# Optimization experiments

Measured on AMD Instinct MI355X. Metric: run time of the kernel, lower is better.

The kernel has to match this reference:

```python
import jax, jax.numpy as jnp
from jax import lax
import numpy as np

B, L_IN, L_OUT, N, COV = 16, 96, 24, 320, 4
E, H = 64, 128
CIN = E + COV


def setup_inputs() -> dict:
    key = jax.random.key(0)
    ks = jax.random.split(key, 16)
    s = 0.05
    inp = {
        'history_data': jax.random.normal(ks[0], (B, L_IN, N, 1 + COV), jnp.float32),
        'future_data': jax.random.normal(ks[1], (B, L_OUT, N, 1 + COV), jnp.float32),
        'We': jax.random.normal(ks[2], (E, 1), jnp.float32) * s,
        'be': jnp.zeros((E,), jnp.float32),
        'Wih0': jax.random.normal(ks[3], (4 * H, CIN), jnp.float32) * s,
        'Whh0': jax.random.normal(ks[4], (4 * H, H), jnp.float32) * s,
        'bih0': jnp.zeros((4 * H,), jnp.float32),
        'bhh0': jnp.zeros((4 * H,), jnp.float32),
        'Wih1': jax.random.normal(ks[5], (4 * H, H), jnp.float32) * s,
        'Whh1': jax.random.normal(ks[6], (4 * H, H), jnp.float32) * s,
        'bih1': jnp.zeros((4 * H,), jnp.float32),
        'bhh1': jnp.zeros((4 * H,), jnp.float32),
        'Wh': jax.random.normal(ks[7], (2, H), jnp.float32) * s,
        'bh': jnp.zeros((2,), jnp.float32),
        'train': 1,
    }
    return inp


def _run_layer(xs, Wih, Whh, bih, bhh):
    # xs: [T, BN, Cin] -> ys: [T, BN, H]
    h0 = jnp.zeros((xs.shape[1], Whh.shape[1]), xs.dtype)

    def step(carry, x):
        h, c = carry
        g = x @ Wih.T + bih + h @ Whh.T + bhh  # [BN, 4H]
        i, f, gg, o = jnp.split(g, 4, axis=-1)  # torch gate order i,f,g,o
        c = jax.nn.sigmoid(f) * c + jax.nn.sigmoid(i) * jnp.tanh(gg)
        h = jax.nn.sigmoid(o) * jnp.tanh(c)
        return (h, c), h

    (_, _), ys = lax.scan(step, (h0, h0), xs)
    return ys


def reference(history_data, future_data, We, be, Wih0, Whh0, bih0, bhh0,
              Wih1, Whh1, bih1, bhh1, Wh, bh, train):
    # train branch (teacher forcing): history_next is always ground truth
    T = L_IN + L_OUT
    tgt = jnp.concatenate([history_data[..., 0:1], future_data[..., 0:1]], axis=1)  # [B,T,N,1]
    cov = jnp.concatenate([history_data[..., 1:], future_data[..., 1:]], axis=1)   # [B,T,N,COV]
    # step t uses target at t-1 and covariates at t, for t = 1..T-1
    embed = tgt[:, :T - 1] @ We.T + be                       # [B,T-1,N,E]
    enc_in = jnp.concatenate([embed, cov[:, 1:T]], axis=-1)  # [B,T-1,N,CIN]
    xs = enc_in.transpose(1, 0, 2, 3).reshape(T - 1, B * N, CIN)
    ys = _run_layer(xs, Wih0, Whh0, bih0, bhh0)
    ys = _run_layer(ys, Wih1, Whh1, bih1, bhh1)
    hid = jax.nn.relu(ys)                                    # [T-1, BN, H]
    head = hid @ Wh.T + bh                                   # [T-1, BN, 2]
    mu = head[..., 0:1]
    sigma = jax.nn.softplus(head[..., 1:2])
    p = jnp.concatenate([mu, sigma], axis=-1)
    p = p[-L_OUT:].reshape(L_OUT, B, N, 2).transpose(1, 0, 2, 3)  # [B,L_out,N,2]
    return p
```

## Files before the change

### kernel.cpp

```cpp
#include <hip/hip_runtime.h>

typedef __bf16 bf16x8 __attribute__((ext_vector_type(8)));
typedef unsigned short us8 __attribute__((ext_vector_type(8)));
typedef float f32x4 __attribute__((ext_vector_type(4)));

#define NROW 32
#define A_STR 136
#define AX_STR 40
#define WL_STR 521
#define NSTEP 119

__device__ __forceinline__ unsigned short f2bf(float f){
  unsigned int x = __builtin_bit_cast(unsigned int, f);
  x += 0x7fffu + ((x >> 16) & 1u);
  return (unsigned short)(x >> 16);
}
__device__ __forceinline__ float bf2f(unsigned short s){
  unsigned int x = ((unsigned int)s) << 16;
  return __builtin_bit_cast(float, x);
}
__device__ __forceinline__ float sigm(float x){ return 1.0f/(1.0f + __expf(-x)); }
__device__ __forceinline__ float tanh_(float x){ float e = __expf(2.0f*x); return 1.0f - 2.0f/(e + 1.0f); }

__device__ __forceinline__ f32x4 MFMA(us8 a, us8 b, f32x4 c){
  return __builtin_amdgcn_mfma_f32_16x16x32_bf16(
      __builtin_bit_cast(bf16x8, a), __builtin_bit_cast(bf16x8, b), c, 0, 0, 0);
}
__device__ __forceinline__ void mfma_ag_first(f32x4& d, us8 a, us8 b){
  asm("s_nop 1\n\tv_mfma_f32_16x16x32_bf16 %0, %1, %2, %0" : "+v"(d) : "v"(a), "a"(b));
}
__device__ __forceinline__ void mfma_ag(f32x4& d, us8 a, us8 b){
  asm("v_mfma_f32_16x16x32_bf16 %0, %1, %2, %0" : "+v"(d) : "v"(a), "a"(b));
}
__device__ __forceinline__ void accfence4(f32x4& a0, f32x4& a1, f32x4& a2, f32x4& a3){
  asm("s_nop 7\n\ts_nop 7\n\ts_nop 2"
      : "+v"(a0), "+v"(a1), "+v"(a2), "+v"(a3));
}

struct SharedMem {
  unsigned short A0[2][NROW*A_STR];
  unsigned short A1[2][NROW*A_STR];
  unsigned short Ax[2][NROW][AX_STR];
  unsigned short xw[512*8];
  unsigned short W0l[8*WL_STR*8];
  float c_lds[2][2][512][4];
  float b1[512];
  float Wh2f[256];
  float red[NROW][16][2];
  float we_s[64];
  float be_s[64];
  float bh_s[2];
};

__global__ __launch_bounds__(512)
__attribute__((amdgpu_waves_per_eu(2, 2)))
void deepar_kernel(
    const float* __restrict__ hist, const float* __restrict__ fut,
    const float* __restrict__ We,   const float* __restrict__ be,
    const float* __restrict__ Wih0, const float* __restrict__ Whh0,
    const float* __restrict__ bih0, const float* __restrict__ bhh0,
    const float* __restrict__ Wih1, const float* __restrict__ Whh1,
    const float* __restrict__ bih1, const float* __restrict__ bhh1,
    const float* __restrict__ Wh,   const float* __restrict__ bh,
    float* __restrict__ out)
{
  __shared__ SharedMem S;
  const int tid = threadIdx.x;
  const int wg  = blockIdx.x;
  const int b   = wg / 10;
  const int n0  = (wg % 10) * NROW;
  const int w   = tid >> 6;
  const int l   = tid & 63;
  const int gq  = l >> 4;
  const int r   = l & 15;
  const int cw  = w * 16;

  {
    us8 z = {0,0,0,0,0,0,0,0};
    us8* pA0 = (us8*)&S.A0[0][0];
    us8* pA1 = (us8*)&S.A1[0][0];
    for (int i = tid; i < 2*NROW*A_STR/8; i += 512){ pA0[i] = z; pA1[i] = z; }
    us8* pAx = (us8*)&S.Ax[0][0][0];
    for (int i = tid; i < 2*NROW*AX_STR/8; i += 512) pAx[i] = z;
    f32x4 zf = {0.f,0.f,0.f,0.f};
    #pragma unroll
    for (int q = 0; q < 4; ++q) *(f32x4*)&S.c_lds[q >> 1][q & 1][tid][0] = zf;
  }
  if (tid < 64)       S.we_s[tid]       = We[tid];
  else if (tid < 128) S.be_s[tid - 64]  = be[tid - 64];
  else if (tid < 384) S.Wh2f[tid - 128] = Wh[tid - 128];
  else if (tid < 386) S.bh_s[tid - 384] = bh[tid - 384];
  __syncthreads();

  {
    const float* wr = Wih0 + tid * 68;
    float u = 0.f, v = 0.f;
    #pragma unroll 8
    for (int e = 0; e < 64; ++e){
      float wv = wr[e];
      u = fmaf(wv, S.we_s[e], u);
      v = fmaf(wv, S.be_s[e], v);
    }
    v += bih0[tid] + bhh0[tid];
    unsigned short* xp = &S.xw[tid * 8];
    xp[0] = f2bf(u);
    xp[1] = f2bf(wr[64]); xp[2] = f2bf(wr[65]); xp[3] = f2bf(wr[66]); xp[4] = f2bf(wr[67]);
    xp[5] = f2bf(v);
    xp[6] = 0; xp[7] = 0;
    S.b1[tid] = bih1[tid] + bhh1[tid];
  }
  for (int idx = tid; idx < 8*512; idx += 512){
    int qgq = idx >> 9, col = idx & 511;
    const float* p = Whh0 + col*128 + qgq*8;
    f32x4 x0 = *(const f32x4*)p;
    f32x4 x1 = *(const f32x4*)(p + 4);
    us8 tt;
    tt[0]=f2bf(x0[0]); tt[1]=f2bf(x0[1]); tt[2]=f2bf(x0[2]); tt[3]=f2bf(x0[3]);
    tt[4]=f2bf(x1[0]); tt[5]=f2bf(x1[1]); tt[6]=f2bf(x1[2]); tt[7]=f2bf(x1[3]);
    *(us8*)&S.W0l[(qgq*WL_STR + col)*8] = tt;
  }
  if (tid < 64){ int row = tid >> 1, bsel = tid & 1; S.Ax[bsel][row][5] = 0x3F80; }
  if (tid < 160){
    int srow, sch, tau;
    if (tid < 32){ srow = tid; sch = 0; tau = 0; }
    else { int k = tid - 32; srow = k >> 2; sch = 1 + (k & 3); tau = 1; }
    const float* p = hist + ((b*96 + tau)*320 + n0 + srow)*5;
    S.Ax[0][srow][sch] = f2bf(p[sch]);
  }

  us8 WV[4][2], WA1[4][4], WA2[4][4];
  #pragma unroll
  for (int m = 0; m < 3; ++m){
    const float* base = (m == 0) ? Whh0 : (m == 1) ? Wih1 : Whh1;
    #pragma unroll
    for (int g = 0; g < 4; ++g){
      int col = g*128 + cw + r;
      #pragma unroll
      for (int q = 0; q < 4; ++q){
        if (m == 0 && q < 2) continue;
        const float* p = base + col*128 + q*32 + gq*8;
        f32x4 x0 = *(const f32x4*)p;
        f32x4 x1 = *(const f32x4*)(p + 4);
        us8 tt;
        tt[0]=f2bf(x0[0]); tt[1]=f2bf(x0[1]); tt[2]=f2bf(x0[2]); tt[3]=f2bf(x0[3]);
        tt[4]=f2bf(x1[0]); tt[5]=f2bf(x1[1]); tt[6]=f2bf(x1[2]); tt[7]=f2bf(x1[3]);
        if (m == 0)      WV[g][q-2] = tt;
        else if (m == 1) WA1[g][q]  = tt;
        else             WA2[g][q]  = tt;
      }
    }
  }

  __syncthreads();

  float b1g[4];
  #pragma unroll
  for (int g = 0; g < 4; ++g) b1g[g] = S.b1[g*128 + cw + r];

  for (int t = 0; t < NSTEP; ++t){
    const int pb = t & 1, nb = pb ^ 1;
    const unsigned short* A0r = S.A0[pb];
    unsigned short*       A0w = S.A0[nb];
    const unsigned short* A1r = S.A1[pb];
    unsigned short*       A1w = S.A1[nb];

    float stv = 0.f; int sto = -1;
    if (t + 1 < NSTEP && tid < 160){
      int srow, sch, tau;
      if (tid < 32){ srow = tid; sch = 0; tau = t + 1; }
      else { int k = tid - 32; srow = k >> 2; sch = 1 + (k & 3); tau = t + 2; }
      const float* p = (tau < 96) ? (hist + ((b*96 + tau)*320 + n0 + srow)*5)
                                  : (fut  + ((b*24 + (tau - 96))*320 + n0 + srow)*5);
      stv = p[sch];
      sto = nb*NROW*AX_STR + srow*AX_STR + sch;
    }

    #pragma unroll
    for (int rt = 0; rt < 2; ++rt){
      const int rbase = rt * 16;
      f32x4 acc[4];
      us8 ax = *(const us8*)&S.Ax[pb][rbase + r][gq*8];
      #pragma unroll
      for (int g = 0; g < 4; ++g){
        us8 bx = *(const us8*)&S.xw[(g*128 + cw + r)*8];
        f32x4 z = {0.f,0.f,0.f,0.f};
        acc[g] = MFMA(ax, bx, z);
      }
      #pragma unroll
      for (int q = 0; q < 2; ++q){
        us8 a = *(const us8*)&A0r[(rbase + r)*A_STR + q*32 + gq*8];
        #pragma unroll
        for (int g = 0; g < 4; ++g){
          us8 bw = *(const us8*)&S.W0l[((q*4 + gq)*WL_STR + g*128 + cw + r)*8];
          acc[g] = MFMA(a, bw, acc[g]);
        }
      }
      #pragma unroll
      for (int q = 2; q < 4; ++q){
        us8 a = *(const us8*)&A0r[(rbase + r)*A_STR + q*32 + gq*8];
        #pragma unroll
        for (int g = 0; g < 4; ++g)
          acc[g] = MFMA(a, WV[g][q-2], acc[g]);
      }
      f32x4 cprev = *(const f32x4*)&S.c_lds[0][rt][tid][0];
      f32x4 cnew;
      #pragma unroll
      for (int j = 0; j < 4; ++j){
        float c = fmaf(sigm(acc[1][j]), cprev[j], sigm(acc[0][j]) * tanh_(acc[2][j]));
        cnew[j] = c;
        float h = sigm(acc[3][j]) * tanh_(c);
        A0w[(rbase + gq*4 + j)*A_STR + cw + r] = f2bf(h);
      }
      *(f32x4*)&S.c_lds[0][rt][tid][0] = cnew;
    }
    __syncthreads();

    #pragma unroll
    for (int rt = 0; rt < 2; ++rt){
      const int rbase = rt * 16;
      f32x4 acc[4];
      #pragma unroll
      for (int g = 0; g < 4; ++g){
        f32x4 iv = {b1g[g], b1g[g], b1g[g], b1g[g]};
        acc[g] = iv;
      }
      {
        us8 a = *(const us8*)&A0w[(rbase + r)*A_STR + 0*32 + gq*8];
        mfma_ag_first(acc[0], a, WA1[0][0]);
        mfma_ag(acc[1], a, WA1[1][0]);
        mfma_ag(acc[2], a, WA1[2][0]);
        mfma_ag(acc[3], a, WA1[3][0]);
      }
      #pragma unroll
      for (int q = 1; q < 4; ++q){
        us8 a = *(const us8*)&A0w[(rbase + r)*A_STR + q*32 + gq*8];
        #pragma unroll
        for (int g = 0; g < 4; ++g) mfma_ag(acc[g], a, WA1[g][q]);
      }
      #pragma unroll
      for (int q = 0; q < 4; ++q){
        us8 a = *(const us8*)&A1r[(rbase + r)*A_STR + q*32 + gq*8];
        #pragma unroll
        for (int g = 0; g < 4; ++g) mfma_ag(acc[g], a, WA2[g][q]);
      }
      accfence4(acc[0], acc[1], acc[2], acc[3]);
      f32x4 cprev = *(const f32x4*)&S.c_lds[1][rt][tid][0];
      f32x4 cnew;
      #pragma unroll
      for (int j = 0; j < 4; ++j){
        float c = fmaf(sigm(acc[1][j]), cprev[j], sigm(acc[0][j]) * tanh_(acc[2][j]));
        cnew[j] = c;
        float h = sigm(acc[3][j]) * tanh_(c);
        A1w[(rbase + gq*4 + j)*A_STR + cw + r] = f2bf(h);
      }
      *(f32x4*)&S.c_lds[1][rt][tid][0] = cnew;
    }
    if (sto >= 0) ((unsigned short*)&S.Ax[0][0][0])[sto] = f2bf(stv);
    __syncthreads();

    if (t >= 95){
      const int rown = tid >> 4, cg = tid & 15;
      us8 hv = *(const us8*)&A1w[rown*A_STR + cg*8];
      f32x4 wA0 = *(const f32x4*)&S.Wh2f[cg*8];
      f32x4 wA1v = *(const f32x4*)&S.Wh2f[cg*8 + 4];
      f32x4 wB0 = *(const f32x4*)&S.Wh2f[128 + cg*8];
      f32x4 wB1 = *(const f32x4*)&S.Wh2f[128 + cg*8 + 4];
      float pm = 0.f, ps = 0.f;
      #pragma unroll
      for (int k = 0; k < 4; ++k){
        float h0v = bf2f(hv[k]);     h0v = h0v > 0.f ? h0v : 0.f;
        float h1v = bf2f(hv[4 + k]); h1v = h1v > 0.f ? h1v : 0.f;
        pm = fmaf(h0v, wA0[k], pm);  pm = fmaf(h1v, wA1v[k], pm);
        ps = fmaf(h0v, wB0[k], ps);  ps = fmaf(h1v, wB1[k], ps);
      }
      S.red[rown][cg][0] = pm; S.red[rown][cg][1] = ps;
      __syncthreads();
      if (tid < 64){
        int row = tid >> 1, o = tid & 1;
        float s = S.bh_s[o];
        #pragma unroll
        for (int k = 0; k < 16; ++k) s += S.red[row][k][o];
        if (o) s = (s > 15.f) ? s : __logf(1.0f + __expf(s));
        out[((b*24 + (t - 95))*320 + (n0 + row))*2 + o] = s;
      }
    }
  }
}

extern "C" void kernel_launch(void* const* d_in, const int* in_sizes, int n_in,
                              void* d_out, int out_size, void* d_ws, size_t ws_size,
                              hipStream_t stream) {
  const float* hist = (const float*)d_in[0];
  const float* fut  = (const float*)d_in[1];
  const float* We   = (const float*)d_in[2];
  const float* be   = (const float*)d_in[3];
  const float* Wih0 = (const float*)d_in[4];
  const float* Whh0 = (const float*)d_in[5];
  const float* bih0 = (const float*)d_in[6];
  const float* bhh0 = (const float*)d_in[7];
  const float* Wih1 = (const float*)d_in[8];
  const float* Whh1 = (const float*)d_in[9];
  const float* bih1 = (const float*)d_in[10];
  const float* bhh1 = (const float*)d_in[11];
  const float* Wh   = (const float*)d_in[12];
  const float* bh   = (const float*)d_in[13];
  float* out = (float*)d_out;

  deepar_kernel<<<dim3(160), dim3(512), 0, stream>>>(
      hist, fut, We, be, Wih0, Whh0, bih0, bhh0,
      Wih1, Whh1, bih1, bhh1, Wh, bh, out);
}
```

Before: 1.107 ms.

## Wavefront-skew LSTM layers to one barrier per step, keep cell state in registers

The two LSTM layers are skewed so that each loop iteration computes layer 0 at step p and layer 1 at step p-1 from the same previous-buffer activations. This halves the number of block-wide barriers per timestep and lets MFMAs from both layers interleave. Cell state moves from LDS into registers, and the output head reduction uses wave shuffles instead of an LDS reduction with an extra barrier. The cost is higher register pressure from two live accumulator sets, plus a prologue and epilogue that add complexity.

New measurement: 3.102 ms. 2.8x slower.

```diff
diff --git a/kernel.cpp b/kernel.cpp
--- a/kernel.cpp
+++ b/kernel.cpp
@@ -43,10 +43,8 @@
   unsigned short Ax[2][NROW][AX_STR];
   unsigned short xw[512*8];
   unsigned short W0l[8*WL_STR*8];
-  float c_lds[2][2][512][4];
   float b1[512];
   float Wh2f[256];
-  float red[NROW][16][2];
   float we_s[64];
   float be_s[64];
   float bh_s[2];
@@ -69,8 +67,8 @@
   const int wg  = blockIdx.x;
   const int b   = wg / 10;
   const int n0  = (wg % 10) * NROW;
+  const int l   = tid & 63;
   const int w   = tid >> 6;
-  const int l   = tid & 63;
   const int gq  = l >> 4;
   const int r   = l & 15;
   const int cw  = w * 16;
@@ -82,9 +80,6 @@
     for (int i = tid; i < 2*NROW*A_STR/8; i += 512){ pA0[i] = z; pA1[i] = z; }
     us8* pAx = (us8*)&S.Ax[0][0][0];
     for (int i = tid; i < 2*NROW*AX_STR/8; i += 512) pAx[i] = z;
-    f32x4 zf = {0.f,0.f,0.f,0.f};
-    #pragma unroll
-    for (int q = 0; q < 4; ++q) *(f32x4*)&S.c_lds[q >> 1][q & 1][tid][0] = zf;
   }
   if (tid < 64)       S.we_s[tid]       = We[tid];
   else if (tid < 128) S.be_s[tid - 64]  = be[tid - 64];
@@ -156,135 +151,179 @@
   float b1g[4];
   #pragma unroll
   for (int g = 0; g < 4; ++g) b1g[g] = S.b1[g*128 + cw + r];
-
-  for (int t = 0; t < NSTEP; ++t){
-    const int pb = t & 1, nb = pb ^ 1;
-    const unsigned short* A0r = S.A0[pb];
-    unsigned short*       A0w = S.A0[nb];
-    const unsigned short* A1r = S.A1[pb];
-    unsigned short*       A1w = S.A1[nb];
-
+  const float bh0 = S.bh_s[0], bh1 = S.bh_s[1];
+
+  f32x4 c0s[2], c1s[2];
+  #pragma unroll
+  for (int rt = 0; rt < 2; ++rt){
+    f32x4 z = {0.f,0.f,0.f,0.f};
+    c0s[rt] = z; c1s[rt] = z;
+  }
+
+  auto head_op = [&](const unsigned short* A1h, int hs){
+    const int rown = tid >> 4, cg = tid & 15;
+    us8 hv = *(const us8*)&A1h[rown*A_STR + cg*8];
+    f32x4 wA0v = *(const f32x4*)&S.Wh2f[cg*8];
+    f32x4 wA1v = *(const f32x4*)&S.Wh2f[cg*8 + 4];
+    f32x4 wB0v = *(const f32x4*)&S.Wh2f[128 + cg*8];
+    f32x4 wB1v = *(const f32x4*)&S.Wh2f[128 + cg*8 + 4];
+    float pm = 0.f, ps = 0.f;
+    #pragma unroll
+    for (int k = 0; k < 4; ++k){
+      float h0v = bf2f(hv[k]);     h0v = h0v > 0.f ? h0v : 0.f;
+      float h1v = bf2f(hv[4 + k]); h1v = h1v > 0.f ? h1v : 0.f;
+      pm = fmaf(h0v, wA0v[k], pm);  pm = fmaf(h1v, wA1v[k], pm);
+      ps = fmaf(h0v, wB0v[k], ps);  ps = fmaf(h1v, wB1v[k], ps);
+    }
+    #pragma unroll
+    for (int m = 1; m < 16; m <<= 1){
+      pm += __shfl_xor(pm, m, 64);
+      ps += __shfl_xor(ps, m, 64);
+    }
+    if (cg == 0){
+      float mu = pm + bh0;
+      float sg = ps + bh1;
+      sg = (sg > 15.f) ? sg : __logf(1.0f + __expf(sg));
+      float2 o2 = make_float2(mu, sg);
+      *(float2*)&out[((b*24 + (hs - 95))*320 + (n0 + rown))*2] = o2;
+    }
+  };
+
+  {
     float stv = 0.f; int sto = -1;
-    if (t + 1 < NSTEP && tid < 160){
+    if (tid < 160){
       int srow, sch, tau;
-      if (tid < 32){ srow = tid; sch = 0; tau = t + 1; }
-      else { int k = tid - 32; srow = k >> 2; sch = 1 + (k & 3); tau = t + 2; }
-      const float* p = (tau < 96) ? (hist + ((b*96 + tau)*320 + n0 + srow)*5)
-                                  : (fut  + ((b*24 + (tau - 96))*320 + n0 + srow)*5);
+      if (tid < 32){ srow = tid; sch = 0; tau = 1; }
+      else { int k = tid - 32; srow = k >> 2; sch = 1 + (k & 3); tau = 2; }
+      const float* p = hist + ((b*96 + tau)*320 + n0 + srow)*5;
       stv = p[sch];
-      sto = nb*NROW*AX_STR + srow*AX_STR + sch;
-    }
-
+      sto = 1*NROW*AX_STR + srow*AX_STR + sch;
+    }
+    unsigned short* A0w = S.A0[0];
     #pragma unroll
     for (int rt = 0; rt < 2; ++rt){
       const int rbase = rt * 16;
       f32x4 acc[4];
-      us8 ax = *(const us8*)&S.Ax[pb][rbase + r][gq*8];
+      us8 ax = *(const us8*)&S.Ax[0][rbase + r][gq*8];
       #pragma unroll
       for (int g = 0; g < 4; ++g){
         us8 bx = *(const us8*)&S.xw[(g*128 + cw + r)*8];
         f32x4 z = {0.f,0.f,0.f,0.f};
         acc[g] = MFMA(ax, bx, z);
       }
-      #pragma unroll
-      for (int q = 0; q < 2; ++q){
-        us8 a = *(const us8*)&A0r[(rbase + r)*A_STR + q*32 + gq*8];
+      f32x4 cn;
+      #pragma unroll
+      for (int j = 0; j < 4; ++j){
+        float c = fmaf(sigm(acc[1][j]), c0s[rt][j], sigm(acc[0][j]) * tanh_(acc[2][j]));
+        cn[j] = c;
+        float h = sigm(acc[3][j]) * tanh_(c);
+        A0w[(rbase + gq*4 + j)*A_STR + cw + r] = f2bf(h);
+      }
+      c0s[rt] = cn;
+    }
+    if (sto >= 0) ((unsigned short*)&S.Ax[0][0][0])[sto] = f2bf(stv);
+    __syncthreads();
+  }
+
+  for (int p = 1; p <= NSTEP; ++p){
+    const int pa = p & 1, pm1 = pa ^ 1;
+    const unsigned short* A0p = S.A0[pm1];
+    unsigned short*       A0w = S.A0[pa];
+    const unsigned short* A1p = S.A1[pa];
+    unsigned short*       A1w = S.A1[pm1];
+    const bool doL0 = (p <= NSTEP - 1);
+
+    float stv = 0.f; int sto = -1;
+    if (p <= NSTEP - 2 && tid < 160){
+      int srow, sch, tau;
+      if (tid < 32){ srow = tid; sch = 0; tau = p + 1; }
+      else { int k = tid - 32; srow = k >> 2; sch = 1 + (k & 3); tau = p + 2; }
+      const float* ptr = (tau < 96) ? (hist + ((b*96 + tau)*320 + n0 + srow)*5)
+                                    : (fut  + ((b*24 + (tau - 96))*320 + n0 + srow)*5);
+      stv = ptr[sch];
+      sto = pm1*NROW*AX_STR + srow*AX_STR + sch;
+    }
+
+    if (p >= 97) head_op(A1p, p - 2);
+
+    #pragma unroll
+    for (int rt = 0; rt < 2; ++rt){
+      const int rbase = rt * 16;
+      f32x4 aL1[4], aL0[4];
+      #pragma unroll
+      for (int g = 0; g < 4; ++g){
+        f32x4 iv = {b1g[g], b1g[g], b1g[g], b1g[g]};
+        aL1[g] = iv;
+      }
+      if (doL0){
+        us8 ax = *(const us8*)&S.Ax[pa][rbase + r][gq*8];
         #pragma unroll
         for (int g = 0; g < 4; ++g){
-          us8 bw = *(const us8*)&S.W0l[((q*4 + gq)*WL_STR + g*128 + cw + r)*8];
-          acc[g] = MFMA(a, bw, acc[g]);
-        }
-      }
-      #pragma unroll
-      for (int q = 2; q < 4; ++q){
-        us8 a = *(const us8*)&A0r[(rbase + r)*A_STR + q*32 + gq*8];
+          us8 bx = *(const us8*)&S.xw[(g*128 + cw + r)*8];
+          f32x4 z = {0.f,0.f,0.f,0.f};
+          aL0[g] = MFMA(ax, bx, z);
+        }
+      }
+      #pragma unroll
+      for (int q = 0; q < 4; ++q){
+        us8 a = *(const us8*)&A0p[(rbase + r)*A_STR + q*32 + gq*8];
+        if (q == 0){
+          mfma_ag_first(aL1[0], a, WA1[0][0]);
+          mfma_ag(aL1[1], a, WA1[1][0]);
+          mfma_ag(aL1[2], a, WA1[2][0]);
+          mfma_ag(aL1[3], a, WA1[3][0]);
+        } else {
+          #pragma unroll
+          for (int g = 0; g < 4; ++g) mfma_ag(aL1[g], a, WA1[g][q]);
+        }
+        if (doL0){
+          if (q < 2){
+            #pragma unroll
+            for (int g = 0; g < 4; ++g){
+              us8 bw = *(const us8*)&S.W0l[((q*4 + gq)*WL_STR + g*128 + cw + r)*8];
+              aL0[g] = MFMA(a, bw, aL0[g]);
+            }
+          } else {
+            #pragma unroll
+            for (int g = 0; g < 4; ++g) aL0[g] = MFMA(a, WV[g][q-2], aL0[g]);
+          }
+        }
+      }
+      #pragma unroll
+      for (int q = 0; q < 4; ++q){
+        us8 a1 = *(const us8*)&A1p[(rbase + r)*A_STR + q*32 + gq*8];
         #pragma unroll
-        for (int g = 0; g < 4; ++g)
-          acc[g] = MFMA(a, WV[g][q-2], acc[g]);
-      }
-      f32x4 cprev = *(const f32x4*)&S.c_lds[0][rt][tid][0];
-      f32x4 cnew;
-      #pragma unroll
-      for (int j = 0; j < 4; ++j){
-        float c = fmaf(sigm(acc[1][j]), cprev[j], sigm(acc[0][j]) * tanh_(acc[2][j]));
-        cnew[j] = c;
-        float h = sigm(acc[3][j]) * tanh_(c);
-        A0w[(rbase + gq*4 + j)*A_STR + cw + r] = f2bf(h);
-      }
-      *(f32x4*)&S.c_lds[0][rt][tid][0] = cnew;
-    }
-    __syncthreads();
-
-    #pragma unroll
-    for (int rt = 0; rt < 2; ++rt){
-      const int rbase = rt * 16;
-      f32x4 acc[4];
-      #pragma unroll
-      for (int g = 0; g < 4; ++g){
-        f32x4 iv = {b1g[g], b1g[g], b1g[g], b1g[g]};
-        acc[g] = iv;
-      }
+        for (int g = 0; g < 4; ++g) mfma_ag(aL1[g], a1, WA2[g][q]);
+      }
+      accfence4(aL1[0], aL1[1], aL1[2], aL1[3]);
       {
-        us8 a = *(const us8*)&A0w[(rbase + r)*A_STR + 0*32 + gq*8];
-        mfma_ag_first(acc[0], a, WA1[0][0]);
-        mfma_ag(acc[1], a, WA1[1][0]);
-        mfma_ag(acc[2], a, WA1[2][0]);
-        mfma_ag(acc[3], a, WA1[3][0]);
-      }
-      #pragma unroll
-      for (int q = 1; q < 4; ++q){
-        us8 a = *(const us8*)&A0w[(rbase + r)*A_STR + q*32 + gq*8];
+        f32x4 cn;
         #pragma unroll
-        for (int g = 0; g < 4; ++g) mfma_ag(acc[g], a, WA1[g][q]);
-      }
-      #pragma unroll
-      for (int q = 0; q < 4; ++q){
-        us8 a = *(const us8*)&A1r[(rbase + r)*A_STR + q*32 + gq*8];
+        for (int j = 0; j < 4; ++j){
+          float c = fmaf(sigm(aL1[1][j]), c1s[rt][j], sigm(aL1[0][j]) * tanh_(aL1[2][j]));
+          cn[j] = c;
+          float h = sigm(aL1[3][j]) * tanh_(c);
+          A1w[(rbase + gq*4 + j)*A_STR + cw + r] = f2bf(h);
+        }
+        c1s[rt] = cn;
+      }
+      if (doL0){
+        f32x4 cn;
         #pragma unroll
-        for (int g = 0; g < 4; ++g) mfma_ag(acc[g], a, WA2[g][q]);
-      }
-      accfence4(acc[0], acc[1], acc[2], acc[3]);
-      f32x4 cprev = *(const f32x4*)&S.c_lds[1][rt][tid][0];
-      f32x4 cnew;
-      #pragma unroll
-      for (int j = 0; j < 4; ++j){
-        float c = fmaf(sigm(acc[1][j]), cprev[j], sigm(acc[0][j]) * tanh_(acc[2][j]));
-        cnew[j] = c;
-        float h = sigm(acc[3][j]) * tanh_(c);
-        A1w[(rbase + gq*4 + j)*A_STR + cw + r] = f2bf(h);
-      }
-      *(f32x4*)&S.c_lds[1][rt][tid][0] = cnew;
+        for (int j = 0; j < 4; ++j){
+          float c = fmaf(sigm(aL0[1][j]), c0s[rt][j], sigm(aL0[0][j]) * tanh_(aL0[2][j]));
+          cn[j] = c;
+          float h = sigm(aL0[3][j]) * tanh_(c);
+          A0w[(rbase + gq*4 + j)*A_STR + cw + r] = f2bf(h);
+        }
+        c0s[rt] = cn;
+      }
     }
     if (sto >= 0) ((unsigned short*)&S.Ax[0][0][0])[sto] = f2bf(stv);
     __syncthreads();
-
-    if (t >= 95){
-      const int rown = tid >> 4, cg = tid & 15;
-      us8 hv = *(const us8*)&A1w[rown*A_STR + cg*8];
-      f32x4 wA0 = *(const f32x4*)&S.Wh2f[cg*8];
-      f32x4 wA1v = *(const f32x4*)&S.Wh2f[cg*8 + 4];
-      f32x4 wB0 = *(const f32x4*)&S.Wh2f[128 + cg*8];
-      f32x4 wB1 = *(const f32x4*)&S.Wh2f[128 + cg*8 + 4];
-      float pm = 0.f, ps = 0.f;
-      #pragma unroll
-      for (int k = 0; k < 4; ++k){
-        float h0v = bf2f(hv[k]);     h0v = h0v > 0.f ? h0v : 0.f;
-        float h1v = bf2f(hv[4 + k]); h1v = h1v > 0.f ? h1v : 0.f;
-        pm = fmaf(h0v, wA0[k], pm);  pm = fmaf(h1v, wA1v[k], pm);
-        ps = fmaf(h0v, wB0[k], ps);  ps = fmaf(h1v, wB1[k], ps);
-      }
-      S.red[rown][cg][0] = pm; S.red[rown][cg][1] = ps;
-      __syncthreads();
-      if (tid < 64){
-        int row = tid >> 1, o = tid & 1;
-        float s = S.bh_s[o];
-        #pragma unroll
-        for (int k = 0; k < 16; ++k) s += S.red[row][k][o];
-        if (o) s = (s > 15.f) ? s : __logf(1.0f + __expf(s));
-        out[((b*24 + (t - 95))*320 + (n0 + row))*2 + o] = s;
-      }
-    }
-  }
+  }
+
+  head_op(S.A1[0], NSTEP - 1);
 }
 
 extern "C" void kernel_launch(void* const* d_in, const int* in_sizes, int n_in,
```
